# Kernel optimization log

Hardware: AMD Instinct MI355X
Metric: run time of the kernel (lower is better)

Reference implementation:

```python
import jax, jax.numpy as jnp
import numpy as np

NUM_EXPERTS = 64
TOPK = 2
N_TOKENS = 16384
DIM = 4096


def setup_inputs() -> dict:
    key = jax.random.key(0)
    k1, k2 = jax.random.split(key)
    x = jax.random.normal(k1, (N_TOKENS, DIM), dtype=jnp.float32)
    # gate weight, torch nn.Linear layout: [num_experts, dim], trunc-normal-ish small init
    W = jax.random.normal(k2, (NUM_EXPERTS, DIM), dtype=jnp.float32) * 0.02
    return {"x": x, "W": W}


def reference(x, W):
    # gate: logits = x @ W^T  -> [N, E]
    router_logits = x @ W.T
    # softmax computed in fp32 (matches dtype=torch.float32 in source)
    routing_weights = jax.nn.softmax(router_logits.astype(jnp.float32), axis=-1)
    # top-k experts per token
    top_w, selected_experts = jax.lax.top_k(routing_weights, TOPK)  # [N, k]
    top_w = top_w.astype(x.dtype)
    sel_flat = selected_experts.reshape(-1)  # [N*k]
    # histogram over experts (torch.histc with bins=num_experts)
    num_tokens_per_expert = jnp.bincount(sel_flat, length=NUM_EXPERTS)
    # stable argsort -> gather (permutation) indices grouping tokens by expert
    gather_indices = jnp.argsort(sel_flat, stable=True)
    return top_w.reshape(-1), gather_indices, num_tokens_per_expert
```

## Files before the change

### kernel.cpp

```cpp
#include <hip/hip_runtime.h>
#include <hip/hip_bf16.h>
#include <math.h>
#include <stdint.h>

#define N_TOKENS 16384
#define DIM 4096
#define NEXP 64

typedef const __attribute__((address_space(1))) void gvoid_t;
typedef __attribute__((address_space(3))) void svoid_t;
typedef short bf16x8 __attribute__((ext_vector_type(8)));
typedef float f32x4 __attribute__((ext_vector_type(4)));

constexpr int TOK_BLK = 32;

__device__ __forceinline__ unsigned short bf16_rn(float f) {
  unsigned u = __float_as_uint(f);
  u += 0x7fffu + ((u >> 16) & 1u);
  return (unsigned short)(u >> 16);
}
__device__ __forceinline__ float bf16_tof(unsigned short h) {
  return __uint_as_float(((unsigned)h) << 16);
}

__device__ __forceinline__ void split8(const float4 a, const float4 b,
                                       bf16x8& hi, bf16x8& lo) {
  const float f[8] = {a.x, a.y, a.z, a.w, b.x, b.y, b.z, b.w};
  union { unsigned u[4]; bf16x8 v; } H, L;
#pragma unroll
  for (int p = 0; p < 4; ++p) {
    const float2 fp = make_float2(f[2 * p], f[2 * p + 1]);
    const __hip_bfloat162 hh = __float22bfloat162_rn(fp);
    const unsigned uh = *(const unsigned*)&hh;
    const float h0 = __uint_as_float(uh << 16);
    const float h1 = __uint_as_float(uh & 0xffff0000u);
    const __hip_bfloat162 ll =
        __float22bfloat162_rn(make_float2(fp.x - h0, fp.y - h1));
    H.u[p] = uh;
    L.u[p] = *(const unsigned*)&ll;
  }
  hi = H.v;
  lo = L.v;
}

__global__ __launch_bounds__(256) void k0_wsplit(const float* __restrict__ W,
                                                 unsigned short* __restrict__ hi,
                                                 unsigned short* __restrict__ lo,
                                                 int* __restrict__ cnt) {
  const int i = (blockIdx.x * 256 + threadIdx.x) * 4;
  const float4 f = *(const float4*)(W + i);
  ushort4 h, l;
  h.x = bf16_rn(f.x); l.x = bf16_rn(f.x - bf16_tof(h.x));
  h.y = bf16_rn(f.y); l.y = bf16_rn(f.y - bf16_tof(h.y));
  h.z = bf16_rn(f.z); l.z = bf16_rn(f.z - bf16_tof(h.z));
  h.w = bf16_rn(f.w); l.w = bf16_rn(f.w - bf16_tof(h.w));
  *(ushort4*)(hi + i) = h;
  *(ushort4*)(lo + i) = l;
  if (blockIdx.x < 8) {
    int4* c4 = (int4*)cnt;
    c4[blockIdx.x * 256 + threadIdx.x] = make_int4(0, 0, 0, 0);
  }
}

__global__ __launch_bounds__(256, 2) void k1_fused(
    const float* __restrict__ x, const unsigned short* __restrict__ Whi,
    const unsigned short* __restrict__ Wlo, float* __restrict__ topw,
    int* __restrict__ sel, int* __restrict__ cnt) {
  __shared__ __align__(16) unsigned char smem[49152 + 256];
  float* const x0 = (float*)smem;
  float* const x1 = (float*)(smem + 8192);
  unsigned short* const wh0 = (unsigned short*)(smem + 16384);
  unsigned short* const wl0 = (unsigned short*)(smem + 24576);
  unsigned short* const wh1 = (unsigned short*)(smem + 32768);
  unsigned short* const wl1 = (unsigned short*)(smem + 40960);
  float* const lg = (float*)smem;
  int* const hist = (int*)(smem + 49152);

  const int tid = threadIdx.x;
  const int lane = tid & 63;
  const int wid = __builtin_amdgcn_readfirstlane(tid >> 6);
  const int th = wid & 1;
  const int eh = wid >> 1;
  const int r = lane & 15;
  const int g = lane >> 4;
  const int tok0 = blockIdx.x * TOK_BLK;

  f32x4 acc[2] = {};

  auto stage = [&](float* xd, unsigned short* whd, unsigned short* wld,
                   int kc) {
#pragma unroll
    for (int q = 0; q < 2; ++q) {
      const int r0 = wid * 8 + q * 4;
      const int row = r0 + (lane >> 4);
      const float* src =
          x + (size_t)(tok0 + row) * DIM + kc + 4 * ((lane & 15) ^ (row & 15));
      __builtin_amdgcn_global_load_lds((gvoid_t*)src, (svoid_t*)(xd + r0 * 64),
                                       16, 0, 0);
    }
#pragma unroll
    for (int q = 0; q < 2; ++q) {
      const int r0 = wid * 16 + q * 8;
      const int row = r0 + (lane >> 3);
      const int s = (lane & 7) ^ (row & 7);
      __builtin_amdgcn_global_load_lds(
          (gvoid_t*)(Whi + (size_t)row * DIM + kc + 8 * s),
          (svoid_t*)(whd + r0 * 64), 16, 0, 0);
      __builtin_amdgcn_global_load_lds(
          (gvoid_t*)(Wlo + (size_t)row * DIM + kc + 8 * s),
          (svoid_t*)(wld + r0 * 64), 16, 0, 0);
    }
  };

  auto compute = [&](const float* xb, const unsigned short* whb,
                     const unsigned short* wlb) {
    const int xrow = th * 16 + r;
#pragma unroll
    for (int h = 0; h < 2; ++h) {
      const int s0 = h * 8 + 2 * g;
      const float4 fa = *(const float4*)(xb + xrow * 64 + 4 * (s0 ^ (xrow & 15)));
      const float4 fb =
          *(const float4*)(xb + xrow * 64 + 4 * ((s0 + 1) ^ (xrow & 15)));
      bf16x8 Ahi, Alo;
      split8(fa, fb, Ahi, Alo);
#pragma unroll
      for (int nt = 0; nt < 2; ++nt) {
        const int wrow = eh * 32 + nt * 16 + r;
        const int wadr = wrow * 64 + 8 * ((h * 4 + g) ^ (wrow & 7));
        const bf16x8 Bhi = *(const bf16x8*)(whb + wadr);
        const bf16x8 Blo = *(const bf16x8*)(wlb + wadr);
        acc[nt] = __builtin_amdgcn_mfma_f32_16x16x32_bf16(Ahi, Bhi, acc[nt], 0, 0, 0);
        acc[nt] = __builtin_amdgcn_mfma_f32_16x16x32_bf16(Alo, Bhi, acc[nt], 0, 0, 0);
        acc[nt] = __builtin_amdgcn_mfma_f32_16x16x32_bf16(Ahi, Blo, acc[nt], 0, 0, 0);
      }
    }
  };

  stage(x0, wh0, wl0, 0);
  for (int t = 0; t < 64; t += 2) {
    if (t + 1 < 64) {
      stage(x1, wh1, wl1, (t + 1) * 64);
      asm volatile("s_waitcnt vmcnt(6)" ::: "memory");
    } else {
      asm volatile("s_waitcnt vmcnt(0)" ::: "memory");
    }
    __builtin_amdgcn_sched_barrier(0);
    __builtin_amdgcn_s_barrier();
    compute(x0, wh0, wl0);
    __builtin_amdgcn_s_barrier();
    __builtin_amdgcn_sched_barrier(0);
    if (t + 2 < 64) {
      stage(x0, wh0, wl0, (t + 2) * 64);
      asm volatile("s_waitcnt vmcnt(6)" ::: "memory");
    } else {
      asm volatile("s_waitcnt vmcnt(0)" ::: "memory");
    }
    __builtin_amdgcn_sched_barrier(0);
    __builtin_amdgcn_s_barrier();
    compute(x1, wh1, wl1);
    __builtin_amdgcn_s_barrier();
    __builtin_amdgcn_sched_barrier(0);
  }

  if (tid < NEXP) hist[tid] = 0;
#pragma unroll
  for (int nt = 0; nt < 2; ++nt)
#pragma unroll
    for (int rg = 0; rg < 4; ++rg)
      lg[(th * 16 + g * 4 + rg) * 68 + eh * 32 + nt * 16 + r] = acc[nt][rg];
  __syncthreads();

  if (tid < TOK_BLK) {
    const float* rowp = lg + tid * 68;
    float4 v[16];
#pragma unroll
    for (int c = 0; c < 16; ++c) v[c] = *(const float4*)(rowp + c * 4);

    float v0 = -INFINITY, v1 = -INFINITY;
    int i0 = 0, i1 = 0;
#define TOP2_STEP(val, idx)                                  \
  {                                                          \
    const float vv = (val);                                  \
    const int ee = (idx);                                    \
    if (vv > v0) { v1 = v0; i1 = i0; v0 = vv; i0 = ee; }     \
    else if (vv > v1) { v1 = vv; i1 = ee; }                  \
  }
#pragma unroll
    for (int c = 0; c < 16; ++c) {
      TOP2_STEP(v[c].x, c * 4 + 0);
      TOP2_STEP(v[c].y, c * 4 + 1);
      TOP2_STEP(v[c].z, c * 4 + 2);
      TOP2_STEP(v[c].w, c * 4 + 3);
    }
#undef TOP2_STEP

    float denom = 0.f;
#pragma unroll
    for (int c = 0; c < 16; ++c) {
      denom += expf(v[c].x - v0);
      denom += expf(v[c].y - v0);
      denom += expf(v[c].z - v0);
      denom += expf(v[c].w - v0);
    }
    const float w0s = 1.0f / denom;
    const float w1s = expf(v1 - v0) / denom;

    const int tk = tok0 + tid;
    topw[2 * tk + 0] = w0s;
    topw[2 * tk + 1] = w1s;
    sel[2 * tk + 0] = i0;
    sel[2 * tk + 1] = i1;
    atomicAdd(&hist[i0], 1);
    atomicAdd(&hist[i1], 1);
  }
  __syncthreads();
  if (tid < NEXP) {
    const int h = hist[tid];
    if (h) atomicAdd(&cnt[tid * 128 + (blockIdx.x >> 2)], h);
  }
}

__global__ void k3_scan(const int* __restrict__ cnt, int* __restrict__ cb,
                        float* __restrict__ counts_out) {
  __shared__ int tot[NEXP];
  const int e = threadIdx.x;
  const int4* row4 = (const int4*)(cnt + e * 128);
  int run = 0;
#pragma unroll
  for (int q = 0; q < 32; ++q) {
    const int4 v = row4[q];
    run += v.x + v.y + v.z + v.w;
  }
  tot[e] = run;
  counts_out[e] = (float)run;
  __syncthreads();
  int g = 0;
  for (int q = 0; q < e; ++q) g += tot[q];
  int r = g;
  for (int p = 0; p < 128; ++p) {
    cb[p * NEXP + e] = r;
    r += cnt[e * 128 + p];
  }
}

__global__ __launch_bounds__(256) void k4_scatter(const int* __restrict__ sel,
                                                  const int* __restrict__ cb,
                                                  float* __restrict__ gout) {
  __shared__ int wcnt[4 * NEXP];
  const int tid = threadIdx.x;
  const int s = blockIdx.x * 256 + tid;
  const int e = sel[s];
  const int lane = tid & 63;
  const int wv = tid >> 6;
  wcnt[tid] = 0;
  __syncthreads();

  unsigned long long mask = ~0ull;
#pragma unroll
  for (int b = 0; b < 6; ++b) {
    const unsigned long long bb = __ballot((e >> b) & 1);
    mask &= ((e >> b) & 1) ? bb : ~bb;
  }
  const unsigned long long below = mask & ((1ull << lane) - 1ull);
  const int wr = __popcll(below);
  if (wr == 0) wcnt[wv * NEXP + e] = __popcll(mask);
  __syncthreads();

  int base = cb[blockIdx.x * NEXP + e];
  for (int w2 = 0; w2 < wv; ++w2) base += wcnt[w2 * NEXP + e];
  gout[base + wr] = (float)s;
}

extern "C" void kernel_launch(void* const* d_in, const int* in_sizes, int n_in,
                              void* d_out, int out_size, void* d_ws, size_t ws_size,
                              hipStream_t stream) {
  const float* x = (const float*)d_in[0];
  const float* W = (const float*)d_in[1];
  float* out = (float*)d_out;

  unsigned short* whi_g = (unsigned short*)d_ws;
  unsigned short* wlo_g = whi_g + NEXP * DIM;
  int* sel = (int*)(wlo_g + NEXP * DIM);
  int* cnt = sel + N_TOKENS * 2;
  int* cb = cnt + 128 * NEXP;

  hipLaunchKernelGGL(k0_wsplit, dim3((NEXP * DIM) / 1024), dim3(256), 0, stream,
                     W, whi_g, wlo_g, cnt);
  hipLaunchKernelGGL(k1_fused, dim3(N_TOKENS / TOK_BLK), dim3(256), 0, stream,
                     x, whi_g, wlo_g, out, sel, cnt);
  hipLaunchKernelGGL(k3_scan, dim3(1), dim3(64), 0, stream, cnt, cb,
                     out + 2 * N_TOKENS + 2 * N_TOKENS);
  hipLaunchKernelGGL(k4_scatter, dim3((2 * N_TOKENS) / 256), dim3(256), 0, stream,
                     sel, cb, out + 2 * N_TOKENS);
}
```

Baseline: 94.68 us.

## Halve token tile in gate GEMM and fold expert scan into scatter kernel

The gate GEMM block now handles 16 tokens instead of 32. Each wave computes one 16-expert tile, shared memory shrinks, and the launch bound targets four blocks per CU for more occupancy and more blocks. The single-block scan kernel is removed: each scatter block now computes its own per-expert prefix offsets from the count table, which saves one launch and a serial one-block step. The cost is redundant scan work in every scatter block and, in the GEMM, weights reloaded from L2 twice as often per token.

Result: no change. 94.23 us (-0.5%).

```diff
diff --git a/kernel.cpp b/kernel.cpp
--- a/kernel.cpp
+++ b/kernel.cpp
@@ -12,7 +12,7 @@
 typedef short bf16x8 __attribute__((ext_vector_type(8)));
 typedef float f32x4 __attribute__((ext_vector_type(4)));
 
-constexpr int TOK_BLK = 32;
+constexpr int TOK_BLK = 16;
 
 __device__ __forceinline__ unsigned short bf16_rn(float f) {
   unsigned u = __float_as_uint(f);
@@ -62,36 +62,33 @@
   }
 }
 
-__global__ __launch_bounds__(256, 2) void k1_fused(
+__global__ __launch_bounds__(256, 4) void k1_fused(
     const float* __restrict__ x, const unsigned short* __restrict__ Whi,
     const unsigned short* __restrict__ Wlo, float* __restrict__ topw,
     int* __restrict__ sel, int* __restrict__ cnt) {
-  __shared__ __align__(16) unsigned char smem[49152 + 256];
+  __shared__ __align__(16) unsigned char smem[40960];
   float* const x0 = (float*)smem;
-  float* const x1 = (float*)(smem + 8192);
-  unsigned short* const wh0 = (unsigned short*)(smem + 16384);
+  float* const x1 = (float*)(smem + 4096);
+  unsigned short* const wh0 = (unsigned short*)(smem + 8192);
+  unsigned short* const wh1 = (unsigned short*)(smem + 16384);
   unsigned short* const wl0 = (unsigned short*)(smem + 24576);
-  unsigned short* const wh1 = (unsigned short*)(smem + 32768);
-  unsigned short* const wl1 = (unsigned short*)(smem + 40960);
+  unsigned short* const wl1 = (unsigned short*)(smem + 32768);
   float* const lg = (float*)smem;
-  int* const hist = (int*)(smem + 49152);
+  int* const hist = (int*)(smem + 4608);
 
   const int tid = threadIdx.x;
   const int lane = tid & 63;
   const int wid = __builtin_amdgcn_readfirstlane(tid >> 6);
-  const int th = wid & 1;
-  const int eh = wid >> 1;
   const int r = lane & 15;
   const int g = lane >> 4;
   const int tok0 = blockIdx.x * TOK_BLK;
 
-  f32x4 acc[2] = {};
+  f32x4 acc = {};
 
   auto stage = [&](float* xd, unsigned short* whd, unsigned short* wld,
                    int kc) {
-#pragma unroll
-    for (int q = 0; q < 2; ++q) {
-      const int r0 = wid * 8 + q * 4;
+    {
+      const int r0 = wid * 4;
       const int row = r0 + (lane >> 4);
       const float* src =
           x + (size_t)(tok0 + row) * DIM + kc + 4 * ((lane & 15) ^ (row & 15));
@@ -114,25 +111,20 @@
 
   auto compute = [&](const float* xb, const unsigned short* whb,
                      const unsigned short* wlb) {
-    const int xrow = th * 16 + r;
 #pragma unroll
     for (int h = 0; h < 2; ++h) {
       const int s0 = h * 8 + 2 * g;
-      const float4 fa = *(const float4*)(xb + xrow * 64 + 4 * (s0 ^ (xrow & 15)));
-      const float4 fb =
-          *(const float4*)(xb + xrow * 64 + 4 * ((s0 + 1) ^ (xrow & 15)));
+      const float4 fa = *(const float4*)(xb + r * 64 + 4 * (s0 ^ r));
+      const float4 fb = *(const float4*)(xb + r * 64 + 4 * ((s0 + 1) ^ r));
       bf16x8 Ahi, Alo;
       split8(fa, fb, Ahi, Alo);
-#pragma unroll
-      for (int nt = 0; nt < 2; ++nt) {
-        const int wrow = eh * 32 + nt * 16 + r;
-        const int wadr = wrow * 64 + 8 * ((h * 4 + g) ^ (wrow & 7));
-        const bf16x8 Bhi = *(const bf16x8*)(whb + wadr);
-        const bf16x8 Blo = *(const bf16x8*)(wlb + wadr);
-        acc[nt] = __builtin_amdgcn_mfma_f32_16x16x32_bf16(Ahi, Bhi, acc[nt], 0, 0, 0);
-        acc[nt] = __builtin_amdgcn_mfma_f32_16x16x32_bf16(Alo, Bhi, acc[nt], 0, 0, 0);
-        acc[nt] = __builtin_amdgcn_mfma_f32_16x16x32_bf16(Ahi, Blo, acc[nt], 0, 0, 0);
-      }
+      const int wrow = wid * 16 + r;
+      const int wadr = wrow * 64 + 8 * ((h * 4 + g) ^ (wrow & 7));
+      const bf16x8 Bhi = *(const bf16x8*)(whb + wadr);
+      const bf16x8 Blo = *(const bf16x8*)(wlb + wadr);
+      acc = __builtin_amdgcn_mfma_f32_16x16x32_bf16(Ahi, Bhi, acc, 0, 0, 0);
+      acc = __builtin_amdgcn_mfma_f32_16x16x32_bf16(Alo, Bhi, acc, 0, 0, 0);
+      acc = __builtin_amdgcn_mfma_f32_16x16x32_bf16(Ahi, Blo, acc, 0, 0, 0);
     }
   };
 
@@ -140,7 +132,7 @@
   for (int t = 0; t < 64; t += 2) {
     if (t + 1 < 64) {
       stage(x1, wh1, wl1, (t + 1) * 64);
-      asm volatile("s_waitcnt vmcnt(6)" ::: "memory");
+      asm volatile("s_waitcnt vmcnt(5)" ::: "memory");
     } else {
       asm volatile("s_waitcnt vmcnt(0)" ::: "memory");
     }
@@ -151,7 +143,7 @@
     __builtin_amdgcn_sched_barrier(0);
     if (t + 2 < 64) {
       stage(x0, wh0, wl0, (t + 2) * 64);
-      asm volatile("s_waitcnt vmcnt(6)" ::: "memory");
+      asm volatile("s_waitcnt vmcnt(5)" ::: "memory");
     } else {
       asm volatile("s_waitcnt vmcnt(0)" ::: "memory");
     }
@@ -164,10 +156,8 @@
 
   if (tid < NEXP) hist[tid] = 0;
 #pragma unroll
-  for (int nt = 0; nt < 2; ++nt)
-#pragma unroll
-    for (int rg = 0; rg < 4; ++rg)
-      lg[(th * 16 + g * 4 + rg) * 68 + eh * 32 + nt * 16 + r] = acc[nt][rg];
+  for (int rg = 0; rg < 4; ++rg)
+    lg[(g * 4 + rg) * 68 + wid * 16 + r] = acc[rg];
   __syncthreads();
 
   if (tid < TOK_BLK) {
@@ -216,57 +206,58 @@
   __syncthreads();
   if (tid < NEXP) {
     const int h = hist[tid];
-    if (h) atomicAdd(&cnt[tid * 128 + (blockIdx.x >> 2)], h);
-  }
-}
-
-__global__ void k3_scan(const int* __restrict__ cnt, int* __restrict__ cb,
-                        float* __restrict__ counts_out) {
-  __shared__ int tot[NEXP];
-  const int e = threadIdx.x;
-  const int4* row4 = (const int4*)(cnt + e * 128);
-  int run = 0;
-#pragma unroll
-  for (int q = 0; q < 32; ++q) {
-    const int4 v = row4[q];
-    run += v.x + v.y + v.z + v.w;
-  }
-  tot[e] = run;
-  counts_out[e] = (float)run;
-  __syncthreads();
-  int g = 0;
-  for (int q = 0; q < e; ++q) g += tot[q];
-  int r = g;
-  for (int p = 0; p < 128; ++p) {
-    cb[p * NEXP + e] = r;
-    r += cnt[e * 128 + p];
-  }
-}
-
-__global__ __launch_bounds__(256) void k4_scatter(const int* __restrict__ sel,
-                                                  const int* __restrict__ cb,
-                                                  float* __restrict__ gout) {
-  __shared__ int wcnt[4 * NEXP];
+    if (h) atomicAdd(&cnt[tid * 128 + (blockIdx.x >> 3)], h);
+  }
+}
+
+__global__ __launch_bounds__(256) void k4_scatter(const int* __restrict__ cnt,
+                                                  const int* __restrict__ sel,
+                                                  float* __restrict__ gout,
+                                                  float* __restrict__ counts_out) {
+  __shared__ int tot[NEXP], parts[NEXP], cbs[NEXP], wcnt[4 * NEXP];
   const int tid = threadIdx.x;
-  const int s = blockIdx.x * 256 + tid;
+  const int b = blockIdx.x;
+  const int s = b * 256 + tid;
   const int e = sel[s];
   const int lane = tid & 63;
   const int wv = tid >> 6;
   wcnt[tid] = 0;
-  __syncthreads();
+
+  if (tid < NEXP) {
+    const int4* row4 = (const int4*)(cnt + tid * 128);
+    int run = 0, part = 0;
+#pragma unroll
+    for (int q = 0; q < 32; ++q) {
+      const int4 v = row4[q];
+      if (4 * q + 0 < b) part += v.x;
+      if (4 * q + 1 < b) part += v.y;
+      if (4 * q + 2 < b) part += v.z;
+      if (4 * q + 3 < b) part += v.w;
+      run += v.x + v.y + v.z + v.w;
+    }
+    tot[tid] = run;
+    parts[tid] = part;
+    if (b == 0) counts_out[tid] = (float)run;
+  }
+  __syncthreads();
+  if (tid < NEXP) {
+    int g2 = 0;
+    for (int q = 0; q < tid; ++q) g2 += tot[q];
+    cbs[tid] = g2 + parts[tid];
+  }
 
   unsigned long long mask = ~0ull;
 #pragma unroll
-  for (int b = 0; b < 6; ++b) {
-    const unsigned long long bb = __ballot((e >> b) & 1);
-    mask &= ((e >> b) & 1) ? bb : ~bb;
+  for (int bb = 0; bb < 6; ++bb) {
+    const unsigned long long bl = __ballot((e >> bb) & 1);
+    mask &= ((e >> bb) & 1) ? bl : ~bl;
   }
   const unsigned long long below = mask & ((1ull << lane) - 1ull);
   const int wr = __popcll(below);
   if (wr == 0) wcnt[wv * NEXP + e] = __popcll(mask);
   __syncthreads();
 
-  int base = cb[blockIdx.x * NEXP + e];
+  int base = cbs[e];
   for (int w2 = 0; w2 < wv; ++w2) base += wcnt[w2 * NEXP + e];
   gout[base + wr] = (float)s;
 }
@@ -282,14 +273,12 @@
   unsigned short* wlo_g = whi_g + NEXP * DIM;
   int* sel = (int*)(wlo_g + NEXP * DIM);
   int* cnt = sel + N_TOKENS * 2;
-  int* cb = cnt + 128 * NEXP;
 
   hipLaunchKernelGGL(k0_wsplit, dim3((NEXP * DIM) / 1024), dim3(256), 0, stream,
                      W, whi_g, wlo_g, cnt);
   hipLaunchKernelGGL(k1_fused, dim3(N_TOKENS / TOK_BLK), dim3(256), 0, stream,
                      x, whi_g, wlo_g, out, sel, cnt);
-  hipLaunchKernelGGL(k3_scan, dim3(1), dim3(64), 0, stream, cnt, cb,
+  hipLaunchKernelGGL(k4_scatter, dim3((2 * N_TOKENS) / 256), dim3(256), 0, stream,
+                     cnt, sel, out + 2 * N_TOKENS,
                      out + 2 * N_TOKENS + 2 * N_TOKENS);
-  hipLaunchKernelGGL(k4_scatter, dim3((2 * N_TOKENS) / 256), dim3(256), 0, stream,
-                     sel, cb, out + 2 * N_TOKENS);
-}
+}
```

## Merge four kernels into one cooperative kernel with grid-wide syncs

Applied to the files above, without the earlier changes.

Replaces the separate W-split, fused GEMM/top-k, scan and scatter launches with a single cooperative kernel. Grid syncs separate the phases. The single-block scan is distributed so each scatter block computes its own prefix offsets from the count table. This removes launch gaps and the serial one-block scan, at the cost of two grid barriers over 512 blocks, which requires all 512 blocks to be co-resident.

After: 182.8 us. 1.93x slower.

```diff
diff --git a/kernel.cpp b/kernel.cpp
--- a/kernel.cpp
+++ b/kernel.cpp
@@ -1,11 +1,14 @@
 #include <hip/hip_runtime.h>
 #include <hip/hip_bf16.h>
+#include <hip/hip_cooperative_groups.h>
 #include <math.h>
 #include <stdint.h>
 
 #define N_TOKENS 16384
 #define DIM 4096
 #define NEXP 64
+
+namespace cg = cooperative_groups;
 
 typedef const __attribute__((address_space(1))) void gvoid_t;
 typedef __attribute__((address_space(3))) void svoid_t;
@@ -43,30 +46,11 @@
   lo = L.v;
 }
 
-__global__ __launch_bounds__(256) void k0_wsplit(const float* __restrict__ W,
-                                                 unsigned short* __restrict__ hi,
-                                                 unsigned short* __restrict__ lo,
-                                                 int* __restrict__ cnt) {
-  const int i = (blockIdx.x * 256 + threadIdx.x) * 4;
-  const float4 f = *(const float4*)(W + i);
-  ushort4 h, l;
-  h.x = bf16_rn(f.x); l.x = bf16_rn(f.x - bf16_tof(h.x));
-  h.y = bf16_rn(f.y); l.y = bf16_rn(f.y - bf16_tof(h.y));
-  h.z = bf16_rn(f.z); l.z = bf16_rn(f.z - bf16_tof(h.z));
-  h.w = bf16_rn(f.w); l.w = bf16_rn(f.w - bf16_tof(h.w));
-  *(ushort4*)(hi + i) = h;
-  *(ushort4*)(lo + i) = l;
-  if (blockIdx.x < 8) {
-    int4* c4 = (int4*)cnt;
-    c4[blockIdx.x * 256 + threadIdx.x] = make_int4(0, 0, 0, 0);
-  }
-}
-
-__global__ __launch_bounds__(256, 2) void k1_fused(
-    const float* __restrict__ x, const unsigned short* __restrict__ Whi,
-    const unsigned short* __restrict__ Wlo, float* __restrict__ topw,
-    int* __restrict__ sel, int* __restrict__ cnt) {
-  __shared__ __align__(16) unsigned char smem[49152 + 256];
+__global__ __launch_bounds__(256, 2) void mono(
+    const float* __restrict__ x, const float* __restrict__ W,
+    float* __restrict__ out, int* __restrict__ sel, int* __restrict__ cnt,
+    unsigned short* __restrict__ Whi, unsigned short* __restrict__ Wlo) {
+  __shared__ __align__(16) unsigned char smem[49408];
   float* const x0 = (float*)smem;
   float* const x1 = (float*)(smem + 8192);
   unsigned short* const wh0 = (unsigned short*)(smem + 16384);
@@ -77,13 +61,31 @@
   int* const hist = (int*)(smem + 49152);
 
   const int tid = threadIdx.x;
+  const int bid = blockIdx.x;
   const int lane = tid & 63;
   const int wid = __builtin_amdgcn_readfirstlane(tid >> 6);
+
+  if (bid < 256) {
+    const int i = (bid * 256 + tid) * 4;
+    const float4 f = *(const float4*)(W + i);
+    ushort4 h, l;
+    h.x = bf16_rn(f.x); l.x = bf16_rn(f.x - bf16_tof(h.x));
+    h.y = bf16_rn(f.y); l.y = bf16_rn(f.y - bf16_tof(h.y));
+    h.z = bf16_rn(f.z); l.z = bf16_rn(f.z - bf16_tof(h.z));
+    h.w = bf16_rn(f.w); l.w = bf16_rn(f.w - bf16_tof(h.w));
+    *(ushort4*)(Whi + i) = h;
+    *(ushort4*)(Wlo + i) = l;
+  } else if (bid < 264) {
+    ((int4*)cnt)[(bid - 256) * 256 + tid] = make_int4(0, 0, 0, 0);
+  }
+  cg::this_grid().sync();
+
   const int th = wid & 1;
   const int eh = wid >> 1;
   const int r = lane & 15;
   const int g = lane >> 4;
-  const int tok0 = blockIdx.x * TOK_BLK;
+  const int tok0 = bid * TOK_BLK;
+  float* const topw = out;
 
   f32x4 acc[2] = {};
 
@@ -216,59 +218,59 @@
   __syncthreads();
   if (tid < NEXP) {
     const int h = hist[tid];
-    if (h) atomicAdd(&cnt[tid * 128 + (blockIdx.x >> 2)], h);
-  }
-}
-
-__global__ void k3_scan(const int* __restrict__ cnt, int* __restrict__ cb,
-                        float* __restrict__ counts_out) {
-  __shared__ int tot[NEXP];
-  const int e = threadIdx.x;
-  const int4* row4 = (const int4*)(cnt + e * 128);
-  int run = 0;
-#pragma unroll
-  for (int q = 0; q < 32; ++q) {
-    const int4 v = row4[q];
-    run += v.x + v.y + v.z + v.w;
-  }
-  tot[e] = run;
-  counts_out[e] = (float)run;
-  __syncthreads();
-  int g = 0;
-  for (int q = 0; q < e; ++q) g += tot[q];
-  int r = g;
-  for (int p = 0; p < 128; ++p) {
-    cb[p * NEXP + e] = r;
-    r += cnt[e * 128 + p];
-  }
-}
-
-__global__ __launch_bounds__(256) void k4_scatter(const int* __restrict__ sel,
-                                                  const int* __restrict__ cb,
-                                                  float* __restrict__ gout) {
-  __shared__ int wcnt[4 * NEXP];
-  const int tid = threadIdx.x;
-  const int s = blockIdx.x * 256 + tid;
-  const int e = sel[s];
-  const int lane = tid & 63;
-  const int wv = tid >> 6;
-  wcnt[tid] = 0;
-  __syncthreads();
-
-  unsigned long long mask = ~0ull;
-#pragma unroll
-  for (int b = 0; b < 6; ++b) {
-    const unsigned long long bb = __ballot((e >> b) & 1);
-    mask &= ((e >> b) & 1) ? bb : ~bb;
-  }
-  const unsigned long long below = mask & ((1ull << lane) - 1ull);
-  const int wr = __popcll(below);
-  if (wr == 0) wcnt[wv * NEXP + e] = __popcll(mask);
-  __syncthreads();
-
-  int base = cb[blockIdx.x * NEXP + e];
-  for (int w2 = 0; w2 < wv; ++w2) base += wcnt[w2 * NEXP + e];
-  gout[base + wr] = (float)s;
+    if (h) atomicAdd(&cnt[tid * 128 + (bid >> 2)], h);
+  }
+  cg::this_grid().sync();
+
+  if (bid < 128) {
+    int* const tot = (int*)smem;
+    int* const parts = (int*)(smem + 256);
+    int* const cbs = (int*)(smem + 512);
+    int* const wcnt = (int*)(smem + 768);
+    const int b = bid;
+    const int s = b * 256 + tid;
+    const int e = sel[s];
+    const int wv = tid >> 6;
+    wcnt[tid] = 0;
+
+    if (tid < NEXP) {
+      const int4* row4 = (const int4*)(cnt + tid * 128);
+      int run = 0, part = 0;
+#pragma unroll
+      for (int q = 0; q < 32; ++q) {
+        const int4 v = row4[q];
+        if (4 * q + 0 < b) part += v.x;
+        if (4 * q + 1 < b) part += v.y;
+        if (4 * q + 2 < b) part += v.z;
+        if (4 * q + 3 < b) part += v.w;
+        run += v.x + v.y + v.z + v.w;
+      }
+      tot[tid] = run;
+      parts[tid] = part;
+      if (b == 0) out[4 * N_TOKENS + tid] = (float)run;
+    }
+    __syncthreads();
+    if (tid < NEXP) {
+      int g2 = 0;
+      for (int q = 0; q < tid; ++q) g2 += tot[q];
+      cbs[tid] = g2 + parts[tid];
+    }
+
+    unsigned long long mask = ~0ull;
+#pragma unroll
+    for (int bb = 0; bb < 6; ++bb) {
+      const unsigned long long bl = __ballot((e >> bb) & 1);
+      mask &= ((e >> bb) & 1) ? bl : ~bl;
+    }
+    const unsigned long long below = mask & ((1ull << lane) - 1ull);
+    const int wr = __popcll(below);
+    if (wr == 0) wcnt[wv * NEXP + e] = __popcll(mask);
+    __syncthreads();
+
+    int base = cbs[e];
+    for (int w2 = 0; w2 < wv; ++w2) base += wcnt[w2 * NEXP + e];
+    out[2 * N_TOKENS + base + wr] = (float)s;
+  }
 }
 
 extern "C" void kernel_launch(void* const* d_in, const int* in_sizes, int n_in,
@@ -282,14 +284,9 @@
   unsigned short* wlo_g = whi_g + NEXP * DIM;
   int* sel = (int*)(wlo_g + NEXP * DIM);
   int* cnt = sel + N_TOKENS * 2;
-  int* cb = cnt + 128 * NEXP;
-
-  hipLaunchKernelGGL(k0_wsplit, dim3((NEXP * DIM) / 1024), dim3(256), 0, stream,
-                     W, whi_g, wlo_g, cnt);
-  hipLaunchKernelGGL(k1_fused, dim3(N_TOKENS / TOK_BLK), dim3(256), 0, stream,
-                     x, whi_g, wlo_g, out, sel, cnt);
-  hipLaunchKernelGGL(k3_scan, dim3(1), dim3(64), 0, stream, cnt, cb,
-                     out + 2 * N_TOKENS + 2 * N_TOKENS);
-  hipLaunchKernelGGL(k4_scatter, dim3((2 * N_TOKENS) / 256), dim3(256), 0, stream,
-                     sel, cb, out + 2 * N_TOKENS);
-}
+
+  void* args[] = {(void*)&x, (void*)&W, (void*)&out, (void*)&sel,
+                  (void*)&cnt, (void*)&whi_g, (void*)&wlo_g};
+  hipLaunchCooperativeKernel((const void*)mono, dim3(N_TOKENS / TOK_BLK),
+                             dim3(256), args, 0, stream);
+}
```
